# Kernel optimization log

Hardware: AMD Instinct MI355X
Metric: run time of the kernel (lower is better)

## Reference

```python
import jax, jax.numpy as jnp
import numpy as np

B, N, D = 2, 2048, 1024
H = 16
DH = D // H

def setup_inputs() -> dict:
    key = jax.random.key(0)
    ks = jax.random.split(key, 9)
    s = 1.0 / np.sqrt(D)
    return {
        "x": jax.random.normal(ks[0], (B, N, D), dtype=jnp.float32),
        "Wq": jax.random.uniform(ks[1], (D, D), jnp.float32, -s, s),
        "bq": jax.random.uniform(ks[2], (D,), jnp.float32, -s, s),
        "Wk": jax.random.uniform(ks[3], (D, D), jnp.float32, -s, s),
        "bk": jax.random.uniform(ks[4], (D,), jnp.float32, -s, s),
        "Wv": jax.random.uniform(ks[5], (D, D), jnp.float32, -s, s),
        "bv": jax.random.uniform(ks[6], (D,), jnp.float32, -s, s),
        "Wo": jax.random.uniform(ks[7], (D, D), jnp.float32, -s, s),
        "bo": jax.random.uniform(ks[8], (D,), jnp.float32, -s, s),
    }

def reference(x, Wq, bq, Wk, bk, Wv, bv, Wo, bo):
    # torch Linear: y = x @ W.T + b
    scale = 1.0 / np.sqrt(DH)
    q = (x @ Wq.T + bq).reshape(B, N, H, DH).transpose(0, 2, 1, 3)  # [B,H,N,DH]
    k = (x @ Wk.T + bk).reshape(B, N, H, DH).transpose(0, 2, 1, 3)
    v = (x @ Wv.T + bv).reshape(B, N, H, DH).transpose(0, 2, 1, 3)
    scores = jnp.einsum('bhnd,bhmd->bhnm', q, k) * scale  # [B,H,N,N]
    attn = jax.nn.softmax(scores, axis=-1)
    out = jnp.einsum('bhnm,bhmd->bhnd', attn, v)  # [B,H,N,DH]
    out = out.transpose(0, 2, 1, 3).reshape(B, N, D)
    return out @ Wo.T + bo
```

## Files before the change

### kernel.cpp

```cpp
#include <hip/hip_runtime.h>
#include <hip/hip_bf16.h>

#define B_  2
#define N_  2048
#define D_  1024
#define H_  16
#define DH_ 64
#define BN_ (B_*N_)

typedef __attribute__((ext_vector_type(8))) short short8;
typedef __attribute__((ext_vector_type(4))) float f32x4;
typedef __attribute__((ext_vector_type(16))) float f32x16;
typedef __attribute__((ext_vector_type(4))) unsigned int uint4v;

typedef __attribute__((address_space(3))) unsigned int lds_u32_t;
typedef const __attribute__((address_space(1))) unsigned int glb_u32_t;

__device__ __forceinline__ void async_load16(const unsigned short* g, unsigned short* l) {
    __builtin_amdgcn_global_load_lds((glb_u32_t*)g, (lds_u32_t*)l, 16, 0, 0);
}

__device__ __forceinline__ unsigned short f2bf(float f) {
    __hip_bfloat16 h = __float2bfloat16(f);
    return *reinterpret_cast<unsigned short*>(&h);
}

__device__ __forceinline__ unsigned int pkbf(float a, float b) {
    unsigned int ua = __float_as_uint(a) + 0x8000u;
    unsigned int ub = __float_as_uint(b) + 0x8000u;
    return __builtin_amdgcn_perm(ub, ua, 0x07060302);
}

#if __has_builtin(__builtin_amdgcn_exp2f)
#define EXP2(x) __builtin_amdgcn_exp2f(x)
#else
#define EXP2(x) exp2f(x)
#endif

#define QSCL 0.1803368801111204f

__global__ __launch_bounds__(256) void cast_kernel(
    const float* __restrict__ x,  const float* __restrict__ wq,
    const float* __restrict__ wk, const float* __restrict__ wv,
    const float* __restrict__ wo,
    unsigned short* __restrict__ xb,  unsigned short* __restrict__ wqb,
    unsigned short* __restrict__ wkb, unsigned short* __restrict__ wvb,
    unsigned short* __restrict__ wob)
{
    const size_t NX = (size_t)BN_ * D_;
    const size_t NW = (size_t)D_ * D_;
    size_t i = ((size_t)blockIdx.x * 256 + threadIdx.x) * 4;
    const float* src; unsigned short* dst; size_t off;
    if (i < NX) { src = x; dst = xb; off = i; }
    else {
        size_t j = (i - NX) >> 20;
        off = (i - NX) & (NW - 1);
        src = (j == 0) ? wq : (j == 1) ? wk : (j == 2) ? wv : wo;
        dst = (j == 0) ? wqb : (j == 1) ? wkb : (j == 2) ? wvb : wob;
    }
    float4 v = *(const float4*)(src + off);
    ushort4 o;
    o.x = f2bf(v.x); o.y = f2bf(v.y); o.z = f2bf(v.z); o.w = f2bf(v.w);
    *(ushort4*)(dst + off) = o;
}

__global__ __launch_bounds__(256, 2) void qkv_fused(
    const unsigned short* __restrict__ xb,
    const unsigned short* __restrict__ wqb, const unsigned short* __restrict__ wkb,
    const unsigned short* __restrict__ wvb,
    const float* __restrict__ bq, const float* __restrict__ bk, const float* __restrict__ bv,
    unsigned short* __restrict__ q, unsigned short* __restrict__ k, unsigned short* __restrict__ vt)
{
    __shared__ __align__(16) unsigned short As[64 * 64];
    __shared__ __align__(16) unsigned short Bq[128 * 64];
    __shared__ __align__(16) unsigned short Bk[128 * 64];
    __shared__ __align__(16) unsigned short Bv[128 * 64];

    const int tid  = threadIdx.x;
    const int lane = tid & 63;
    const int wave = tid >> 6;
    const int l15 = lane & 15, quad = lane >> 4;

    const int p  = blockIdx.x & 3, hh = blockIdx.x >> 2;
    const int bx = p * 2 + (blockIdx.y & 1);
    const int by = hh * 32 + (blockIdx.y >> 1);
    const int row0 = by * 64, col0 = bx * 128;

    const int srow = lane >> 3, scb = lane & 7;

    f32x4 aq[4][2] = {}, ak[4][2] = {}, av[4][2] = {};

    for (int k0 = 0; k0 < D_; k0 += 64) {
        __syncthreads();
#pragma unroll
        for (int cc = 0; cc < 2; ++cc) {
            int c  = wave * 2 + cc;
            int lr = c * 8 + srow;
            int gcol = k0 + ((scb ^ (lr & 7)) * 8);
            async_load16(xb + (size_t)(row0 + lr) * D_ + gcol, As + c * 512);
        }
#pragma unroll
        for (int cc = 0; cc < 4; ++cc) {
            int c  = wave * 4 + cc;
            int lr = c * 8 + srow;
            int gcol = k0 + ((scb ^ (lr & 7)) * 8);
            size_t off = (size_t)(col0 + lr) * D_ + gcol;
            async_load16(wqb + off, Bq + c * 512);
            async_load16(wkb + off, Bk + c * 512);
            async_load16(wvb + off, Bv + c * 512);
        }
        __syncthreads();

#pragma unroll
        for (int kf = 0; kf < 2; ++kf) {
            const int swz = ((kf * 4 + quad) ^ (l15 & 7)) * 8;
            short8 af[4];
#pragma unroll
            for (int mi = 0; mi < 4; mi++)
                af[mi] = *(const short8*)(&As[(mi * 16 + l15) * 64 + swz]);
#pragma unroll
            for (int ni = 0; ni < 2; ni++) {
                const int boff = (wave * 32 + ni * 16 + l15) * 64 + swz;
                short8 fq = *(const short8*)(&Bq[boff]);
                short8 fk = *(const short8*)(&Bk[boff]);
                short8 fv = *(const short8*)(&Bv[boff]);
#pragma unroll
                for (int mi = 0; mi < 4; mi++) {
                    aq[mi][ni] = __builtin_amdgcn_mfma_f32_16x16x32_bf16(af[mi], fq, aq[mi][ni], 0, 0, 0);
                    ak[mi][ni] = __builtin_amdgcn_mfma_f32_16x16x32_bf16(af[mi], fk, ak[mi][ni], 0, 0, 0);
                    av[mi][ni] = __builtin_amdgcn_mfma_f32_16x16x32_bf16(af[mi], fv, av[mi][ni], 0, 0, 0);
                }
            }
        }
    }

    __syncthreads();
#pragma unroll
    for (int ni = 0; ni < 2; ni++) {
        int c = wave * 32 + ni * 16 + l15;
        float biq = bq[col0 + c], bik = bk[col0 + c], biv = bv[col0 + c];
#pragma unroll
        for (int mi = 0; mi < 4; mi++) {
            int r4 = mi * 16 + quad * 4;
            ushort4 pv;
            pv.x = f2bf(av[mi][ni][0] + biv);
            pv.y = f2bf(av[mi][ni][1] + biv);
            pv.z = f2bf(av[mi][ni][2] + biv);
            pv.w = f2bf(av[mi][ni][3] + biv);
            *(ushort4*)(Bv + c * 64 + (r4 ^ ((c & 7) << 3))) = pv;
#pragma unroll
            for (int r = 0; r < 4; r++) {
                int row = r4 + r;
                int sc  = c ^ ((row & 7) << 3);
                Bq[row * 128 + sc] = f2bf((aq[mi][ni][r] + biq) * QSCL);
                Bk[row * 128 + sc] = f2bf(ak[mi][ni][r] + bik);
            }
        }
    }
    __syncthreads();
#pragma unroll
    for (int itx = 0; itx < 4; ++itx) {
        int item = itx * 256 + tid;
        int row = item >> 4, cb = item & 15;
        uint4v vq = *(const uint4v*)(Bq + row * 128 + ((cb ^ (row & 7)) * 8));
        *(uint4v*)(q + (size_t)(row0 + row) * D_ + col0 + cb * 8) = vq;
        uint4v vk = *(const uint4v*)(Bk + row * 128 + ((cb ^ (row & 7)) * 8));
        *(uint4v*)(k + (size_t)(row0 + row) * D_ + col0 + cb * 8) = vk;
        int c = item >> 3, rb = item & 7;
        uint4v vv = *(const uint4v*)(Bv + c * 64 + ((rb ^ (c & 7)) * 8));
        *(uint4v*)(vt + (size_t)(col0 + c) * BN_ + row0 + rb * 8) = vv;
    }
}

template<int OUT_MODE>
__device__ __forceinline__ void gemm_body(
    unsigned short* __restrict__ As, unsigned short* __restrict__ Bs,
    const unsigned short* __restrict__ A, const unsigned short* __restrict__ W,
    const float* __restrict__ bias, void* __restrict__ Cout, int bx, int by)
{
    constexpr int K = D_;
    const int tid  = threadIdx.x;
    const int lane = tid & 63;
    const int wave = tid >> 6;
    const int l15 = lane & 15, quad = lane >> 4;

    f32x4 acc[4][2] = {};
    const int row0 = by * 64, col0 = bx * 128;

    const int srow = lane >> 3;
    const int scb  = lane & 7;

    for (int k0 = 0; k0 < K; k0 += 64) {
        __syncthreads();
#pragma unroll
        for (int cc = 0; cc < 2; ++cc) {
            int c  = wave * 2 + cc;
            int lr = c * 8 + srow;
            int gcol = k0 + ((scb ^ (lr & 7)) * 8);
            async_load16(A + (size_t)(row0 + lr) * K + gcol, As + c * 512);
        }
#pragma unroll
        for (int cc = 0; cc < 4; ++cc) {
            int c  = wave * 4 + cc;
            int lr = c * 8 + srow;
            int gcol = k0 + ((scb ^ (lr & 7)) * 8);
            async_load16(W + (size_t)(col0 + lr) * K + gcol, Bs + c * 512);
        }
        __syncthreads();

#pragma unroll
        for (int kf = 0; kf < 2; ++kf) {
            const int swz = ((kf * 4 + quad) ^ (l15 & 7)) * 8;
            short8 af[4], bf[2];
#pragma unroll
            for (int mi = 0; mi < 4; mi++)
                af[mi] = *(const short8*)(&As[(mi * 16 + l15) * 64 + swz]);
#pragma unroll
            for (int ni = 0; ni < 2; ni++)
                bf[ni] = *(const short8*)(&Bs[(wave * 32 + ni * 16 + l15) * 64 + swz]);
#pragma unroll
            for (int mi = 0; mi < 4; mi++)
#pragma unroll
                for (int ni = 0; ni < 2; ni++)
                    acc[mi][ni] = __builtin_amdgcn_mfma_f32_16x16x32_bf16(
                        af[mi], bf[ni], acc[mi][ni], 0, 0, 0);
        }
    }

#pragma unroll
    for (int ni = 0; ni < 2; ni++) {
        int col = col0 + wave * 32 + ni * 16 + l15;
        float bvv = bias[col];
#pragma unroll
        for (int mi = 0; mi < 4; mi++) {
            int row = row0 + mi * 16 + quad * 4;
#pragma unroll
            for (int r = 0; r < 4; r++)
                ((float*)Cout)[(size_t)(row + r) * D_ + col] = acc[mi][ni][r] + bvv;
        }
    }
}

__device__ __forceinline__ void xcd_swz(int& bx, int& by) {
    int w = blockIdx.y * 8 + blockIdx.x;
    int s = (w & 7) * 64 + (w >> 3);
    bx = s & 7; by = s >> 3;
}

__global__ __launch_bounds__(256, 5) void out_gemm(
    const unsigned short* __restrict__ attn, const unsigned short* __restrict__ wob,
    const float* __restrict__ bo, float* __restrict__ out)
{
    __shared__ __align__(16) unsigned short As[64 * 64];
    __shared__ __align__(16) unsigned short Bs[128 * 64];
    int bx, by; xcd_swz(bx, by);
    gemm_body<0>(As, Bs, attn, wob, bo, out, bx, by);
}

__global__ __launch_bounds__(256) void attn_kernel(
    const unsigned short* __restrict__ q, const unsigned short* __restrict__ k,
    const unsigned short* __restrict__ vt, unsigned short* __restrict__ o)
{
    __shared__ __align__(16) unsigned short Ks[2][64 * 64];
    __shared__ __align__(16) unsigned short Vs[2][64 * 64];

    const int tid = threadIdx.x;
    const int lane = tid & 63, wave = tid >> 6;
    const int l31 = lane & 31, kq = lane >> 5;
    const int bh = blockIdx.x;
    const int qt = blockIdx.y;
    const int b = bh >> 4, h = bh & 15;

    const unsigned short* qb = q  + (size_t)b * N_ * D_ + h * DH_;
    const unsigned short* kb = k  + (size_t)b * N_ * D_ + h * DH_;
    const unsigned short* vb = vt + (size_t)h * DH_ * BN_ + (size_t)b * N_;

    const int qrow0 = qt * 128 + wave * 32;

    short8 qf[4];
#pragma unroll
    for (int s = 0; s < 4; s++)
        qf[s] = *(const short8*)(qb + (size_t)(qrow0 + l31) * D_ + s * 16 + kq * 8);

    f32x16 oacc[2] = {};
    float lsum = 0.f;

    const int srow = lane >> 3, scb = lane & 7;

    auto stage = [&](int bi, int kv0) {
#pragma unroll
        for (int cc = 0; cc < 2; ++cc) {
            int c  = wave * 2 + cc;
            int lr = c * 8 + srow;
            int swz8 = (scb ^ (lr & 7)) * 8;
            async_load16(kb + (size_t)(kv0 + lr) * D_ + swz8, (unsigned short*)Ks[bi] + c * 512);
            async_load16(vb + (size_t)lr * BN_ + kv0 + swz8,  (unsigned short*)Vs[bi] + c * 512);
        }
    };

    stage(0, 0);

    const int NIT = N_ / 64;
    for (int it = 0; it < NIT; ++it) {
        const int cur = it & 1;
        __syncthreads();
        if (it + 1 < NIT) stage(cur ^ 1, (it + 1) * 64);

        const unsigned short* Kc = Ks[cur];
        const unsigned short* Vc = Vs[cur];

        f32x16 st[2] = {};
        __builtin_amdgcn_s_setprio(1);
#pragma unroll
        for (int s = 0; s < 4; s++) {
#pragma unroll
            for (int mb = 0; mb < 2; mb++) {
                short8 kfr = *(const short8*)((const char*)Kc +
                    (mb * 32 + l31) * 128 + (((2 * s + kq) ^ (l31 & 7)) * 16));
                st[mb] = __builtin_amdgcn_mfma_f32_32x32x16_bf16(
                    kfr, qf[s], st[mb], 0, 0, 0);
            }
        }
        __builtin_amdgcn_s_setprio(0);

#pragma unroll
        for (int mb = 0; mb < 2; mb++) {
            unsigned int pk[8];
#pragma unroll
            for (int g = 0; g < 4; g++) {
                float p0 = EXP2(st[mb][g * 4 + 0]);
                float p1 = EXP2(st[mb][g * 4 + 1]);
                float p2 = EXP2(st[mb][g * 4 + 2]);
                float p3 = EXP2(st[mb][g * 4 + 3]);
                lsum += (p0 + p1) + (p2 + p3);
                pk[2 * g + 0] = pkbf(p0, p1);
                pk[2 * g + 1] = pkbf(p2, p3);
            }
            __builtin_amdgcn_s_setprio(1);
#pragma unroll
            for (int s = 0; s < 2; s++) {
                uint4v fu;
                fu[0] = pk[4 * s + 0]; fu[1] = pk[4 * s + 1];
                fu[2] = pk[4 * s + 2]; fu[3] = pk[4 * s + 3];
                short8 pf = __builtin_bit_cast(short8, fu);
                const int blkA = 4 * mb + 2 * s;
#pragma unroll
                for (int nb = 0; nb < 2; nb++) {
                    const char* vrow = (const char*)Vc + (nb * 32 + l31) * 128;
                    uint2 vlo = *(const uint2*)(vrow + ((blkA       ^ (l31 & 7)) * 16) + kq * 8);
                    uint2 vhi = *(const uint2*)(vrow + (((blkA + 1) ^ (l31 & 7)) * 16) + kq * 8);
                    uint4v vu; vu[0] = vlo.x; vu[1] = vlo.y; vu[2] = vhi.x; vu[3] = vhi.y;
                    short8 vf = __builtin_bit_cast(short8, vu);
                    oacc[nb] = __builtin_amdgcn_mfma_f32_32x32x16_bf16(
                        pf, vf, oacc[nb], 0, 0, 0);
                }
            }
            __builtin_amdgcn_s_setprio(0);
        }
    }

    lsum += __shfl_xor(lsum, 32);
    __syncthreads();
    float* Lt = (float*)&Ks[0][0] + wave * 32;
    if (kq == 0) Lt[l31] = lsum;
    asm volatile("s_waitcnt lgkmcnt(0)" ::: "memory");

#pragma unroll
    for (int g = 0; g < 4; g++)
#pragma unroll
        for (int rr = 0; rr < 4; rr++) {
            int reg = g * 4 + rr;
            float inv = 1.f / Lt[rr + 8 * g + 4 * kq];
            int row = qrow0 + rr + 8 * g + 4 * kq;
            size_t base = ((size_t)b * N_ + row) * D_ + h * DH_;
#pragma unroll
            for (int nb = 0; nb < 2; nb++)
                o[base + nb * 32 + l31] = f2bf(oacc[nb][reg] * inv);
        }
}

extern "C" void kernel_launch(void* const* d_in, const int* in_sizes, int n_in,
                              void* d_out, int out_size, void* d_ws, size_t ws_size,
                              hipStream_t stream)
{
    const float* x  = (const float*)d_in[0];
    const float* Wq = (const float*)d_in[1];
    const float* bq = (const float*)d_in[2];
    const float* Wk = (const float*)d_in[3];
    const float* bk = (const float*)d_in[4];
    const float* Wv = (const float*)d_in[5];
    const float* bv = (const float*)d_in[6];
    const float* Wo = (const float*)d_in[7];
    const float* bo = (const float*)d_in[8];
    float* out = (float*)d_out;

    char* ws = (char*)d_ws;
    unsigned short* xb  = (unsigned short*)(ws + 0);
    unsigned short* wqb = (unsigned short*)(ws + 8388608);
    unsigned short* wkb = (unsigned short*)(ws + 10485760);
    unsigned short* wvb = (unsigned short*)(ws + 12582912);
    unsigned short* wob = (unsigned short*)(ws + 14680064);
    unsigned short* qd  = (unsigned short*)(ws + 16777216);
    unsigned short* kd  = (unsigned short*)(ws + 25165824);
    unsigned short* vtd = (unsigned short*)(ws + 33554432);
    unsigned short* ad  = (unsigned short*)(ws + 41943040);

    cast_kernel<<<8192, 256, 0, stream>>>(x, Wq, Wk, Wv, Wo, xb, wqb, wkb, wvb, wob);
    qkv_fused<<<dim3(8, 64), 256, 0, stream>>>(xb, wqb, wkb, wvb, bq, bk, bv, qd, kd, vtd);
    attn_kernel<<<dim3(32, 16), 256, 0, stream>>>(qd, kd, vtd, ad);
    out_gemm<<<dim3(8, 64), 256, 0, stream>>>(ad, wob, bo, out);
}
```

Measured before the change: 191.2 us.

## Split KV sequence across two wave groups in attention block and merge partials

The attention block grows from 4 to 8 waves. Each half of the block processes half of the key/value sequence for the same 128 query rows, then the two halves merge their output accumulators and row sums through LDS before normalization and store. The aim is more waves per CU to hide latency and a shorter serial KV loop per wave. In exchange, the double-buffered prefetch is replaced by a load, sync, compute, sync pattern with no overlap, and the merge adds LDS traffic and extra barriers.

```diff
diff --git a/kernel.cpp b/kernel.cpp
--- a/kernel.cpp
+++ b/kernel.cpp
@@ -257,16 +257,19 @@
     gemm_body<0>(As, Bs, attn, wob, bo, out, bx, by);
 }
 
-__global__ __launch_bounds__(256) void attn_kernel(
+__global__ __launch_bounds__(512, 4) void attn_kernel(
     const unsigned short* __restrict__ q, const unsigned short* __restrict__ k,
     const unsigned short* __restrict__ vt, unsigned short* __restrict__ o)
 {
     __shared__ __align__(16) unsigned short Ks[2][64 * 64];
     __shared__ __align__(16) unsigned short Vs[2][64 * 64];
+    __shared__ float Ls[4][32];
 
     const int tid = threadIdx.x;
     const int lane = tid & 63, wave = tid >> 6;
     const int l31 = lane & 31, kq = lane >> 5;
+    const int wlow = wave & 3;
+    const int half = wave >> 2;
     const int bh = blockIdx.x;
     const int qt = blockIdx.y;
     const int b = bh >> 4, h = bh & 15;
@@ -275,7 +278,7 @@
     const unsigned short* kb = k  + (size_t)b * N_ * D_ + h * DH_;
     const unsigned short* vb = vt + (size_t)h * DH_ * BN_ + (size_t)b * N_;
 
-    const int qrow0 = qt * 128 + wave * 32;
+    const int qrow0 = qt * 128 + wlow * 32;
 
     short8 qf[4];
 #pragma unroll
@@ -286,28 +289,25 @@
     float lsum = 0.f;
 
     const int srow = lane >> 3, scb = lane & 7;
-
-    auto stage = [&](int bi, int kv0) {
-#pragma unroll
-        for (int cc = 0; cc < 2; ++cc) {
-            int c  = wave * 2 + cc;
-            int lr = c * 8 + srow;
-            int swz8 = (scb ^ (lr & 7)) * 8;
-            async_load16(kb + (size_t)(kv0 + lr) * D_ + swz8, (unsigned short*)Ks[bi] + c * 512);
-            async_load16(vb + (size_t)lr * BN_ + kv0 + swz8,  (unsigned short*)Vs[bi] + c * 512);
-        }
-    };
-
-    stage(0, 0);
-
-    const int NIT = N_ / 64;
+    const int kvoff = half * (N_ / 2);
+
+    const int NIT = 16;
     for (int it = 0; it < NIT; ++it) {
-        const int cur = it & 1;
-        __syncthreads();
-        if (it + 1 < NIT) stage(cur ^ 1, (it + 1) * 64);
-
-        const unsigned short* Kc = Ks[cur];
-        const unsigned short* Vc = Vs[cur];
+        {
+            const int kv0 = kvoff + it * 64;
+#pragma unroll
+            for (int cc = 0; cc < 2; ++cc) {
+                int c  = wlow * 2 + cc;
+                int lr = c * 8 + srow;
+                int swz8 = (scb ^ (lr & 7)) * 8;
+                async_load16(kb + (size_t)(kv0 + lr) * D_ + swz8, (unsigned short*)Ks[half] + c * 512);
+                async_load16(vb + (size_t)lr * BN_ + kv0 + swz8,  (unsigned short*)Vs[half] + c * 512);
+            }
+        }
+        __syncthreads();
+
+        const unsigned short* Kc = Ks[half];
+        const unsigned short* Vc = Vs[half];
 
         f32x16 st[2] = {};
         __builtin_amdgcn_s_setprio(1);
@@ -357,26 +357,56 @@
             }
             __builtin_amdgcn_s_setprio(0);
         }
+        __syncthreads();
     }
 
     lsum += __shfl_xor(lsum, 32);
+
+    const int idx = wave & 3;
+    float* mrg = ((idx & 2) ? (float*)Vs : (float*)Ks) + (idx & 1) * 2048;
+
+    if (wave >= 4) {
+#pragma unroll
+        for (int q8 = 0; q8 < 8; ++q8) {
+            int nb = q8 >> 2, j = (q8 & 3) * 4;
+            f32x4 c;
+            c[0] = oacc[nb][j + 0]; c[1] = oacc[nb][j + 1];
+            c[2] = oacc[nb][j + 2]; c[3] = oacc[nb][j + 3];
+            *(f32x4*)(mrg + (q8 * 64 + lane) * 4) = c;
+        }
+        if (kq == 0) Ls[wave - 4][l31] = lsum;
+    }
     __syncthreads();
-    float* Lt = (float*)&Ks[0][0] + wave * 32;
-    if (kq == 0) Lt[l31] = lsum;
-    asm volatile("s_waitcnt lgkmcnt(0)" ::: "memory");
-
-#pragma unroll
-    for (int g = 0; g < 4; g++)
-#pragma unroll
-        for (int rr = 0; rr < 4; rr++) {
-            int reg = g * 4 + rr;
-            float inv = 1.f / Lt[rr + 8 * g + 4 * kq];
-            int row = qrow0 + rr + 8 * g + 4 * kq;
-            size_t base = ((size_t)b * N_ + row) * D_ + h * DH_;
-#pragma unroll
-            for (int nb = 0; nb < 2; nb++)
-                o[base + nb * 32 + l31] = f2bf(oacc[nb][reg] * inv);
-        }
+    if (wave < 4) {
+#pragma unroll
+        for (int q8 = 0; q8 < 8; ++q8) {
+            int nb = q8 >> 2, j = (q8 & 3) * 4;
+            f32x4 r = *(const f32x4*)(mrg + (q8 * 64 + lane) * 4);
+            oacc[nb][j + 0] += r[0]; oacc[nb][j + 1] += r[1];
+            oacc[nb][j + 2] += r[2]; oacc[nb][j + 3] += r[3];
+        }
+        lsum += Ls[wave][l31];
+    }
+    __syncthreads();
+
+    if (wave < 4) {
+        float* Lt = (float*)&Ks[0][0] + wave * 32;
+        if (kq == 0) Lt[l31] = lsum;
+        asm volatile("s_waitcnt lgkmcnt(0)" ::: "memory");
+
+#pragma unroll
+        for (int g = 0; g < 4; g++)
+#pragma unroll
+            for (int rr = 0; rr < 4; rr++) {
+                int reg = g * 4 + rr;
+                float inv = 1.f / Lt[rr + 8 * g + 4 * kq];
+                int row = qrow0 + rr + 8 * g + 4 * kq;
+                size_t base = ((size_t)b * N_ + row) * D_ + h * DH_;
+#pragma unroll
+                for (int nb = 0; nb < 2; nb++)
+                    o[base + nb * 32 + l31] = f2bf(oacc[nb][reg] * inv);
+            }
+    }
 }
 
 extern "C" void kernel_launch(void* const* d_in, const int* in_sizes, int n_in,
@@ -407,6 +437,6 @@
 
     cast_kernel<<<8192, 256, 0, stream>>>(x, Wq, Wk, Wv, Wo, xb, wqb, wkb, wvb, wob);
     qkv_fused<<<dim3(8, 64), 256, 0, stream>>>(xb, wqb, wkb, wvb, bq, bk, bv, qd, kd, vtd);
-    attn_kernel<<<dim3(32, 16), 256, 0, stream>>>(qd, kd, vtd, ad);
+    attn_kernel<<<dim3(32, 16), 512, 0, stream>>>(qd, kd, vtd, ad);
     out_gemm<<<dim3(8, 64), 256, 0, stream>>>(ad, wob, bo, out);
 }
```

Result: faster. 184.1 us (-3.7%).
